# Performance work log

Measured on AMD Instinct MI355X. Metric: run time of the kernel, lower is better.

Reference implementation:

```python
import jax, jax.numpy as jnp
import numpy as np

B, C, H, W = 4, 256, 64, 64
CI = C // 2  # inter_channels = in_channels // 2
BN_EPS = 1e-5


def setup_inputs() -> dict:
    key = jax.random.key(0)
    ks = jax.random.split(key, 13)
    s = 0.02  # weight init scale for stability
    inp = {
        "x": jax.random.normal(ks[0], (B, C, H, W), dtype=jnp.float32),
        "w_theta": jax.random.normal(ks[1], (CI, C), dtype=jnp.float32) * s,
        "b_theta": jax.random.normal(ks[2], (CI,), dtype=jnp.float32) * s,
        "w_phi": jax.random.normal(ks[3], (CI, C), dtype=jnp.float32) * s,
        "b_phi": jax.random.normal(ks[4], (CI,), dtype=jnp.float32) * s,
        "w_g": jax.random.normal(ks[5], (CI, C), dtype=jnp.float32) * s,
        "b_g": jax.random.normal(ks[6], (CI,), dtype=jnp.float32) * s,
        "w_out": jax.random.normal(ks[7], (C, CI), dtype=jnp.float32) * s,
        "b_out": jax.random.normal(ks[8], (C,), dtype=jnp.float32) * s,
        "bn_gamma": jax.random.normal(ks[9], (C,), dtype=jnp.float32),
        "bn_beta": jax.random.normal(ks[10], (C,), dtype=jnp.float32) * s,
        "bn_mean": jax.random.normal(ks[11], (C,), dtype=jnp.float32) * s,
        "bn_var": jax.random.uniform(ks[12], (C,), dtype=jnp.float32, minval=0.5, maxval=1.5),
    }
    return inp


def _conv1x1(x, w, b):
    # 1x1 conv == channel contraction. x: [B,C,H,W], w: [O,C], b: [O]
    return jnp.einsum("bchw,oc->bohw", x, w) + b[None, :, None, None]


def reference(x, w_theta, b_theta, w_phi, b_phi, w_g, b_g,
              w_out, b_out, bn_gamma, bn_beta, bn_mean, bn_var):
    b, c, h, w = x.shape
    n = h * w
    # projections, flattened over spatial positions
    theta = _conv1x1(x, w_theta, b_theta).reshape(b, CI, n).transpose(0, 2, 1)  # [B,N,Ci]
    phi = _conv1x1(x, w_phi, b_phi).reshape(b, CI, n)                            # [B,Ci,N]
    g = _conv1x1(x, w_g, b_g).reshape(b, CI, n).transpose(0, 2, 1)               # [B,N,Ci]
    # unscaled dot-product attention over all spatial positions
    f = jnp.einsum("bnc,bcm->bnm", theta, phi)   # [B,N,N]
    attn = jax.nn.softmax(f, axis=-1)
    y = jnp.einsum("bnm,bmc->bnc", attn, g)      # [B,N,Ci]
    y = y.transpose(0, 2, 1).reshape(b, CI, h, w)
    # output 1x1 conv + BatchNorm (inference form) + residual
    wy = _conv1x1(y, w_out, b_out)
    inv = (bn_gamma / jnp.sqrt(bn_var + BN_EPS))[None, :, None, None]
    wy = (wy - bn_mean[None, :, None, None]) * inv + bn_beta[None, :, None, None]
    return wy + x
```

## Files before the change

kernel.cpp:

```cpp
#include <hip/hip_runtime.h>
#include <stdint.h>

#define NPOS 4096
#define NCH  256
#define NCI  128
#define NBATCH 4
#define NSPLIT 4
#define KRANGE (NPOS / NSPLIT)
#define LOG2E 1.44269504f

typedef float f32x16 __attribute__((ext_vector_type(16)));
typedef short short8 __attribute__((ext_vector_type(8)));

static __device__ __forceinline__ uint16_t f2bf(float f) {
  uint32_t u = __float_as_uint(f);
  u += 0x7fff + ((u >> 16) & 1);
  return (uint16_t)(u >> 16);
}
static __device__ __forceinline__ float bf2f(uint16_t h) {
  return __uint_as_float(((uint32_t)h) << 16);
}
static __device__ __forceinline__ uint32_t cvtpk(float a, float b) {
  uint32_t r;
  asm("v_cvt_pk_bf16_f32 %0, %1, %2" : "=v"(r) : "v"(a), "v"(b));
  return r;
}

__global__ void prep_kernel(const float* __restrict__ w_theta,
                            const float* __restrict__ w_phi,
                            const float* __restrict__ w_g,
                            const float* __restrict__ w_out,
                            const float* __restrict__ b_theta,
                            const float* __restrict__ b_phi,
                            const float* __restrict__ b_g,
                            const float* __restrict__ b_out,
                            const float* __restrict__ bn_gamma,
                            const float* __restrict__ bn_beta,
                            const float* __restrict__ bn_mean,
                            const float* __restrict__ bn_var,
                            uint16_t* __restrict__ w_all,
                            uint16_t* __restrict__ w_out_bf,
                            float* __restrict__ b_all,
                            float* __restrict__ bn_scale,
                            float* __restrict__ bn_shift) {
  int idx = blockIdx.x * 256 + threadIdx.x;
  if (idx < 98304) {
    int o = idx >> 8;
    float v;
    if (o < 128)      v = w_theta[idx] * LOG2E;
    else if (o < 256) v = w_phi[idx - 32768];
    else              v = w_g[idx - 65536];
    w_all[idx] = f2bf(v);
  } else if (idx < 131072) {
    w_out_bf[idx - 98304] = f2bf(w_out[idx - 98304]);
  } else if (idx < 131456) {
    int o = idx - 131072;
    float v = (o < 128) ? b_theta[o] * LOG2E
            : (o < 256) ? b_phi[o - 128] : b_g[o - 256];
    b_all[o] = v;
  } else if (idx < 131712) {
    int o = idx - 131456;
    float s = bn_gamma[o] * rsqrtf(bn_var[o] + 1e-5f);
    bn_scale[o] = s;
    bn_shift[o] = (b_out[o] - bn_mean[o]) * s + bn_beta[o];
  }
}

__global__ __launch_bounds__(512) void proj_kernel(
    const float* __restrict__ x, const uint16_t* __restrict__ w_all,
    const float* __restrict__ b_all,
    uint16_t* __restrict__ Q, uint16_t* __restrict__ K,
    uint16_t* __restrict__ Vt) {
  __shared__ __align__(16) uint16_t xs[64 * 256];
  int b = blockIdx.y;
  int n0 = blockIdx.x * 64;
  int tid = threadIdx.x;
  int lane = tid & 63;
  int wv = tid >> 6;
  const float* xb = x + ((size_t)b * NCH) * NPOS + n0;
  #pragma unroll
  for (int i = 0; i < 16; i++) {
    int c = wv * 32 + i * 2;
    float v0 = xb[(size_t)c * NPOS + lane];
    float v1 = xb[(size_t)(c + 1) * NPOS + lane];
    uint32_t u = cvtpk(v0, v1);
    *(uint32_t*)((char*)xs + lane * 512 + ((2 * c) ^ ((lane & 7) << 4))) = u;
  }
  __syncthreads();

  int l31 = lane & 31;
  int h2 = lane >> 5;
  int nt = wv & 1;
  int og = wv >> 1;
  int nl = nt * 32 + l31;
  int swz = (nl & 7) << 4;

  f32x16 accQ, accK, accV;
  #pragma unroll
  for (int i = 0; i < 16; i++) { accQ[i] = 0.f; accK[i] = 0.f; accV[i] = 0.f; }

  const uint16_t* wt = w_all + (size_t)(og * 32 + l31) * 256 + h2 * 8;
  const uint16_t* wp = wt + 128 * 256;
  const uint16_t* wg = wt + 256 * 256;

  #pragma unroll
  for (int kc = 0; kc < 16; kc++) {
    int c2 = kc * 32 + h2 * 16;
    short8 xf = *(const short8*)((const char*)xs + nl * 512 + (c2 ^ swz));
    short8 a = *(const short8*)(wt + kc * 16);
    short8 p = *(const short8*)(wp + kc * 16);
    short8 g = *(const short8*)(wg + kc * 16);
    accQ = __builtin_amdgcn_mfma_f32_32x32x16_bf16(xf, a, accQ, 0, 0, 0);
    accK = __builtin_amdgcn_mfma_f32_32x32x16_bf16(xf, p, accK, 0, 0, 0);
    accV = __builtin_amdgcn_mfma_f32_32x32x16_bf16(g, xf, accV, 0, 0, 0);
  }

  int ocol = og * 32 + l31;
  float bq = b_all[ocol];
  float bk = b_all[128 + ocol];
  #pragma unroll
  for (int r = 0; r < 16; r++) {
    int n = nt * 32 + (r & 3) + 8 * (r >> 2) + 4 * h2;
    size_t row = ((size_t)b * NPOS + n0 + n) * NCI + ocol;
    Q[row] = f2bf(accQ[r] + bq);
    K[row] = f2bf(accK[r] + bk);
  }
  #pragma unroll
  for (int r = 0; r < 16; r++) {
    int ci = og * 32 + (r & 3) + 8 * (r >> 2) + 4 * h2;
    Vt[((size_t)b * NCI + ci) * NPOS + n0 + nt * 32 + l31] =
        f2bf(accV[r] + b_all[256 + ci]);
  }
}

__global__ __launch_bounds__(256, 2) void attn_kernel(
    const uint16_t* __restrict__ Q, const uint16_t* __restrict__ K,
    const uint16_t* __restrict__ Vt, uint16_t* __restrict__ Ypart,
    float* __restrict__ Dpart) {
  __shared__ __align__(16) uint16_t kv[4 * 4096];
  uint16_t* Kb0 = kv;
  uint16_t* Vb0 = kv + 4096;
  uint16_t* Kb1 = kv + 8192;
  uint16_t* Vb1 = kv + 12288;

  int wg = blockIdx.x;
  int xcd = wg & 7;
  int slot = wg >> 3;
  int b = xcd >> 1;
  int split = (xcd & 1) * 2 + (slot & 1);
  int qblk = slot >> 1;
  int tid = threadIdx.x;
  int lane = tid & 63;
  int wv = tid >> 6;
  int q32 = lane & 31;
  int h2 = lane >> 5;
  int qb = qblk * 128 + wv * 32;

  const uint16_t* Qb = Q + ((size_t)b * NPOS + qb + q32) * NCI + h2 * 8;
  short8 qf[8];
  #pragma unroll
  for (int kc = 0; kc < 8; kc++)
    qf[kc] = *reinterpret_cast<const short8*>(Qb + kc * 16);

  const uint16_t* Kg = K + (size_t)b * NPOS * NCI;
  const uint16_t* Vg = Vt + (size_t)b * NCI * NPOS;

  int posA = wv * 2048 + lane * 16;
  int posB = posA + 1024;
  int rKA = posA >> 8, cKA = (posA >> 4) & 15;
  int rKB = posB >> 8, cKB = (posB >> 4) & 15;
  int wrKA = rKA * 128 + ((cKA ^ (rKA & 7)) << 3);
  int wrKB = rKB * 128 + ((cKB ^ (rKB & 7)) << 3);
  int gKA = rKA * NCI + cKA * 8;
  int gKB = rKB * NCI + cKB * 8;
  int ciA = posA >> 6, vsA = (posA >> 4) & 3;
  int ciB = posB >> 6, vsB = (posB >> 4) & 3;
  int wrVA = ciA * 32 + ((vsA ^ ((ciA >> 1) & 3)) << 3);
  int wrVB = ciB * 32 + ((vsB ^ ((ciB >> 1) & 3)) << 3);
  int gVA = ciA * NPOS + vsA * 8;
  int gVB = ciB * NPOS + vsB * 8;

  short8 stK0, stK1, stV0, stV1;

#define LOADR(MB)                                                             \
  {                                                                           \
    const uint16_t* kt = Kg + (size_t)(MB) * NCI;                             \
    const uint16_t* vt = Vg + (MB);                                           \
    stK0 = *(const short8*)(kt + gKA);                                        \
    stK1 = *(const short8*)(kt + gKB);                                        \
    stV0 = *(const short8*)(vt + gVA);                                        \
    stV1 = *(const short8*)(vt + gVB);                                        \
  }
#define WRITE(KB, VB)                                                         \
  {                                                                           \
    *(short8*)((KB) + wrKA) = stK0;                                           \
    *(short8*)((KB) + wrKB) = stK1;                                           \
    *(short8*)((VB) + wrVA) = stV0;                                           \
    *(short8*)((VB) + wrVB) = stV1;                                           \
  }

  f32x16 yacc[4];
  #pragma unroll
  for (int d = 0; d < 4; d++)
    #pragma unroll
    for (int i = 0; i < 16; i++) yacc[d][i] = 0.f;

  float den = 0.f;
  int m0 = split * KRANGE;

#define ATTN_BODY(KB, VB)                                                     \
  {                                                                           \
    short8 kf[8];                                                             \
    _Pragma("unroll")                                                         \
    for (int kc = 0; kc < 8; kc++) {                                          \
      int off = q32 * 128 + (((2 * kc + h2) ^ (q32 & 7)) << 3);               \
      kf[kc] = *(const short8*)((KB) + off);                                  \
    }                                                                         \
    short8 vf[2][4];                                                          \
    _Pragma("unroll")                                                         \
    for (int kc2 = 0; kc2 < 2; kc2++)                                         \
      _Pragma("unroll")                                                       \
      for (int dt = 0; dt < 4; dt++) {                                        \
        int ci = q32 + dt * 32;                                               \
        int off = ci * 32 + (((2 * kc2 + h2) ^ ((q32 >> 1) & 3)) << 3);       \
        vf[kc2][dt] = *(const short8*)((VB) + off);                           \
      }                                                                       \
    f32x16 s;                                                                 \
    _Pragma("unroll")                                                         \
    for (int i = 0; i < 16; i++) s[i] = 0.f;                                  \
    _Pragma("unroll")                                                         \
    for (int kc = 0; kc < 8; kc++)                                            \
      s = __builtin_amdgcn_mfma_f32_32x32x16_bf16(kf[kc], qf[kc], s, 0, 0, 0);\
    _Pragma("unroll")                                                         \
    for (int i = 0; i < 16; i++) s[i] = exp2f(s[i]);                          \
    float r0 = (s[0] + s[1]) + (s[2] + s[3]);                                 \
    float r1 = (s[4] + s[5]) + (s[6] + s[7]);                                 \
    float r2 = (s[8] + s[9]) + (s[10] + s[11]);                               \
    float r3 = (s[12] + s[13]) + (s[14] + s[15]);                             \
    den += (r0 + r1) + (r2 + r3);                                             \
    uint32_t pk[8];                                                           \
    _Pragma("unroll")                                                         \
    for (int a2 = 0; a2 < 4; a2++) {                                          \
      pk[a2 * 2]     = cvtpk(s[4 * a2],     s[4 * a2 + 1]);                   \
      pk[a2 * 2 + 1] = cvtpk(s[4 * a2 + 2], s[4 * a2 + 3]);                   \
    }                                                                         \
    _Pragma("unroll")                                                         \
    for (int kc2 = 0; kc2 < 2; kc2++) {                                       \
      uint32_t A0 = pk[4 * kc2],     B0 = pk[4 * kc2 + 2];                    \
      uint32_t A1 = pk[4 * kc2 + 1], B1 = pk[4 * kc2 + 3];                    \
      asm("v_permlane32_swap_b32 %0, %1" : "+v"(A0), "+v"(B0));               \
      asm("v_permlane32_swap_b32 %0, %1" : "+v"(A1), "+v"(B1));               \
      union { short8 v; uint32_t u[4]; } pb;                                  \
      pb.u[0] = A0;                                                           \
      pb.u[1] = A1;                                                           \
      pb.u[2] = B0;                                                           \
      pb.u[3] = B1;                                                           \
      _Pragma("unroll")                                                       \
      for (int dt = 0; dt < 4; dt++)                                          \
        yacc[dt] = __builtin_amdgcn_mfma_f32_32x32x16_bf16(vf[kc2][dt], pb.v, \
                                                           yacc[dt], 0, 0, 0);\
    }                                                                         \
  }

  LOADR(m0)
  WRITE(Kb0, Vb0)
  __syncthreads();

  for (int it = 0; it < 16; it++) {
    int ms = it * 64;
    LOADR(m0 + ms + 32)
    ATTN_BODY(Kb0, Vb0)
    WRITE(Kb1, Vb1)
    __syncthreads();
    int mn = m0 + ((ms + 64) & (KRANGE - 1));
    LOADR(mn)
    ATTN_BODY(Kb1, Vb1)
    WRITE(Kb0, Vb0)
    __syncthreads();
  }
#undef ATTN_BODY
#undef LOADR
#undef WRITE

  size_t pbase = ((size_t)(b * NSPLIT + split)) * NCI * NPOS;
  #pragma unroll
  for (int dt = 0; dt < 4; dt++)
    #pragma unroll
    for (int r = 0; r < 16; r++) {
      int drow = dt * 32 + (r & 3) + 8 * (r >> 2) + 4 * h2;
      Ypart[pbase + (size_t)drow * NPOS + qb + q32] = f2bf(yacc[dt][r]);
    }
  den += __shfl_xor(den, 32);
  if (h2 == 0) {
    size_t sbase = (size_t)(b * NSPLIT + split) * NPOS + qb + q32;
    Dpart[sbase] = den;
  }
}

__global__ __launch_bounds__(512) void out_kernel(
    const uint16_t* __restrict__ Yp, const float* __restrict__ Dp,
    const uint16_t* __restrict__ w_out_bf,
    const float* __restrict__ bn_scale, const float* __restrict__ bn_shift,
    const float* __restrict__ x, float* __restrict__ out) {
  __shared__ __align__(16) uint16_t ys[64 * 128];
  int b = blockIdx.y;
  int n0 = blockIdx.x * 64;
  int tid = threadIdx.x;
  int n = tid & 63;
  int wv = tid >> 6;

  float den = 0.f;
  #pragma unroll
  for (int s2 = 0; s2 < NSPLIT; s2++)
    den += Dp[(size_t)(b * NSPLIT + s2) * NPOS + n0 + n];
  float rden = 1.f / den;

  #pragma unroll
  for (int i = 0; i < 16; i += 2) {
    int ci0 = wv * 16 + i;
    float a0 = 0.f, a1 = 0.f;
    #pragma unroll
    for (int s2 = 0; s2 < NSPLIT; s2++) {
      size_t base = ((size_t)(b * NSPLIT + s2) * NCI) * NPOS + n0 + n;
      a0 += bf2f(Yp[base + (size_t)ci0 * NPOS]);
      a1 += bf2f(Yp[base + (size_t)(ci0 + 1) * NPOS]);
    }
    *(uint32_t*)((char*)ys + n * 256 + ((2 * ci0) ^ ((n & 7) << 4))) =
        cvtpk(a0 * rden, a1 * rden);
  }
  __syncthreads();

  int lane = tid & 63;
  int l31 = lane & 31;
  int h2 = lane >> 5;
  int og = wv;
  f32x16 acc0, acc1;
  #pragma unroll
  for (int i = 0; i < 16; i++) { acc0[i] = 0.f; acc1[i] = 0.f; }
  const uint16_t* wo_base = w_out_bf + (size_t)(og * 32 + l31) * NCI + h2 * 8;
  int swz = (l31 & 7) << 4;
  #pragma unroll
  for (int kc = 0; kc < 8; kc++) {
    int c2 = kc * 32 + h2 * 16;
    short8 wo = *(const short8*)(wo_base + kc * 16);
    short8 y0 = *(const short8*)((const char*)ys + l31 * 256 + (c2 ^ swz));
    short8 y1 = *(const short8*)((const char*)ys + (32 + l31) * 256 + (c2 ^ swz));
    acc0 = __builtin_amdgcn_mfma_f32_32x32x16_bf16(wo, y0, acc0, 0, 0, 0);
    acc1 = __builtin_amdgcn_mfma_f32_32x32x16_bf16(wo, y1, acc1, 0, 0, 0);
  }
  #pragma unroll
  for (int r = 0; r < 16; r++) {
    int o = og * 32 + (r & 3) + 8 * (r >> 2) + 4 * h2;
    float sc = bn_scale[o];
    float sh = bn_shift[o];
    size_t base = ((size_t)b * NCH + o) * NPOS + n0;
    out[base + l31]      = fmaf(acc0[r], sc, sh) + x[base + l31];
    out[base + 32 + l31] = fmaf(acc1[r], sc, sh) + x[base + 32 + l31];
  }
}

extern "C" void kernel_launch(void* const* d_in, const int* in_sizes, int n_in,
                              void* d_out, int out_size, void* d_ws, size_t ws_size,
                              hipStream_t stream) {
  const float* x        = (const float*)d_in[0];
  const float* w_theta  = (const float*)d_in[1];
  const float* b_theta  = (const float*)d_in[2];
  const float* w_phi    = (const float*)d_in[3];
  const float* b_phi    = (const float*)d_in[4];
  const float* w_g      = (const float*)d_in[5];
  const float* b_g      = (const float*)d_in[6];
  const float* w_out    = (const float*)d_in[7];
  const float* b_out    = (const float*)d_in[8];
  const float* bn_gamma = (const float*)d_in[9];
  const float* bn_beta  = (const float*)d_in[10];
  const float* bn_mean  = (const float*)d_in[11];
  const float* bn_var   = (const float*)d_in[12];

  char* ws = (char*)d_ws;
  uint16_t* w_all    = (uint16_t*)ws;  ws += (size_t)384 * 256 * 2;
  uint16_t* w_out_bf = (uint16_t*)ws;  ws += (size_t)256 * 128 * 2;
  float* b_all       = (float*)ws;     ws += 2048;
  float* bn_scale    = (float*)ws;     ws += 1024;
  float* bn_shift    = (float*)ws;     ws += 1024;
  uint16_t* Q   = (uint16_t*)ws;  ws += (size_t)NBATCH * NPOS * NCI * 2;
  uint16_t* Kb  = (uint16_t*)ws;  ws += (size_t)NBATCH * NPOS * NCI * 2;
  uint16_t* Vt  = (uint16_t*)ws;  ws += (size_t)NBATCH * NCI * NPOS * 2;
  uint16_t* Yp  = (uint16_t*)ws;  ws += (size_t)NBATCH * NSPLIT * NCI * NPOS * 2;
  float* Dp     = (float*)ws;     ws += (size_t)NBATCH * NSPLIT * NPOS * 4;

  hipLaunchKernelGGL(prep_kernel, dim3(515), dim3(256), 0, stream,
                     w_theta, w_phi, w_g, w_out, b_theta, b_phi, b_g, b_out,
                     bn_gamma, bn_beta, bn_mean, bn_var,
                     w_all, w_out_bf, b_all, bn_scale, bn_shift);
  hipLaunchKernelGGL(proj_kernel, dim3(64, NBATCH), dim3(512), 0, stream,
                     x, w_all, b_all, Q, Kb, Vt);
  hipLaunchKernelGGL(attn_kernel, dim3(512), dim3(256), 0, stream,
                     Q, Kb, Vt, Yp, Dp);
  hipLaunchKernelGGL(out_kernel, dim3(64, NBATCH), dim3(512), 0, stream,
                     Yp, Dp, w_out_bf, bn_scale, bn_shift, x, (float*)d_out);
}
```

Before: 156.9 us.

## Double key splits, raise attention occupancy, and vectorize partial reduction

Splits the key range of each batch's attention into 8 chunks instead of 4, doubling the attention grid and requesting 4 workgroups per CU via launch bounds. Wave priority is raised around the MFMA/softmax section to favor compute over loads. The output kernel now reduces the partial results with 16-byte vector loads, one channel row per thread group, and computes reciprocal denominators once into shared memory. This trades twice the partial-result memory traffic, and possible register spilling under the tighter register limit, for better latency hiding.

```diff
diff --git a/kernel.cpp b/kernel.cpp
--- a/kernel.cpp
+++ b/kernel.cpp
@@ -5,7 +5,7 @@
 #define NCH  256
 #define NCI  128
 #define NBATCH 4
-#define NSPLIT 4
+#define NSPLIT 8
 #define KRANGE (NPOS / NSPLIT)
 #define LOG2E 1.44269504f
 
@@ -133,7 +133,7 @@
   }
 }
 
-__global__ __launch_bounds__(256, 2) void attn_kernel(
+__global__ __launch_bounds__(256, 4) void attn_kernel(
     const uint16_t* __restrict__ Q, const uint16_t* __restrict__ K,
     const uint16_t* __restrict__ Vt, uint16_t* __restrict__ Ypart,
     float* __restrict__ Dpart) {
@@ -147,8 +147,8 @@
   int xcd = wg & 7;
   int slot = wg >> 3;
   int b = xcd >> 1;
-  int split = (xcd & 1) * 2 + (slot & 1);
-  int qblk = slot >> 1;
+  int split = (xcd & 1) * 4 + (slot & 3);
+  int qblk = slot >> 2;
   int tid = threadIdx.x;
   int lane = tid & 63;
   int wv = tid >> 6;
@@ -225,6 +225,7 @@
         int off = ci * 32 + (((2 * kc2 + h2) ^ ((q32 >> 1) & 3)) << 3);       \
         vf[kc2][dt] = *(const short8*)((VB) + off);                           \
       }                                                                       \
+    __builtin_amdgcn_s_setprio(1);                                            \
     f32x16 s;                                                                 \
     _Pragma("unroll")                                                         \
     for (int i = 0; i < 16; i++) s[i] = 0.f;                                  \
@@ -260,13 +261,14 @@
         yacc[dt] = __builtin_amdgcn_mfma_f32_32x32x16_bf16(vf[kc2][dt], pb.v, \
                                                            yacc[dt], 0, 0, 0);\
     }                                                                         \
+    __builtin_amdgcn_s_setprio(0);                                            \
   }
 
   LOADR(m0)
   WRITE(Kb0, Vb0)
   __syncthreads();
 
-  for (int it = 0; it < 16; it++) {
+  for (int it = 0; it < KRANGE / 64; it++) {
     int ms = it * 64;
     LOADR(m0 + ms + 32)
     ATTN_BODY(Kb0, Vb0)
@@ -303,34 +305,49 @@
     const float* __restrict__ bn_scale, const float* __restrict__ bn_shift,
     const float* __restrict__ x, float* __restrict__ out) {
   __shared__ __align__(16) uint16_t ys[64 * 128];
+  __shared__ float rden_s[64];
   int b = blockIdx.y;
   int n0 = blockIdx.x * 64;
   int tid = threadIdx.x;
-  int n = tid & 63;
+
+  if (tid < 64) {
+    float den = 0.f;
+    #pragma unroll
+    for (int s2 = 0; s2 < NSPLIT; s2++)
+      den += Dp[(size_t)(b * NSPLIT + s2) * NPOS + n0 + tid];
+    rden_s[tid] = 1.f / den;
+  }
+  __syncthreads();
+
+  {
+    int ci = tid >> 2;
+    int g = tid & 3;
+    float sum[16];
+    #pragma unroll
+    for (int j = 0; j < 16; j++) sum[j] = 0.f;
+    #pragma unroll
+    for (int s2 = 0; s2 < NSPLIT; s2++) {
+      const uint16_t* p =
+          Yp + ((size_t)(b * NSPLIT + s2) * NCI + ci) * NPOS + n0 + g * 16;
+      short8 v0 = *(const short8*)(p);
+      short8 v1 = *(const short8*)(p + 8);
+      #pragma unroll
+      for (int j = 0; j < 8; j++) {
+        sum[j]     += bf2f((uint16_t)v0[j]);
+        sum[8 + j] += bf2f((uint16_t)v1[j]);
+      }
+    }
+    #pragma unroll
+    for (int j = 0; j < 16; j++) {
+      int n = g * 16 + j;
+      float v = sum[j] * rden_s[n];
+      *(uint16_t*)((char*)ys + n * 256 + ((2 * ci) ^ ((n & 7) << 4))) = f2bf(v);
+    }
+  }
+  __syncthreads();
+
+  int lane = tid & 63;
   int wv = tid >> 6;
-
-  float den = 0.f;
-  #pragma unroll
-  for (int s2 = 0; s2 < NSPLIT; s2++)
-    den += Dp[(size_t)(b * NSPLIT + s2) * NPOS + n0 + n];
-  float rden = 1.f / den;
-
-  #pragma unroll
-  for (int i = 0; i < 16; i += 2) {
-    int ci0 = wv * 16 + i;
-    float a0 = 0.f, a1 = 0.f;
-    #pragma unroll
-    for (int s2 = 0; s2 < NSPLIT; s2++) {
-      size_t base = ((size_t)(b * NSPLIT + s2) * NCI) * NPOS + n0 + n;
-      a0 += bf2f(Yp[base + (size_t)ci0 * NPOS]);
-      a1 += bf2f(Yp[base + (size_t)(ci0 + 1) * NPOS]);
-    }
-    *(uint32_t*)((char*)ys + n * 256 + ((2 * ci0) ^ ((n & 7) << 4))) =
-        cvtpk(a0 * rden, a1 * rden);
-  }
-  __syncthreads();
-
-  int lane = tid & 63;
   int l31 = lane & 31;
   int h2 = lane >> 5;
   int og = wv;
@@ -394,7 +411,7 @@
                      w_all, w_out_bf, b_all, bn_scale, bn_shift);
   hipLaunchKernelGGL(proj_kernel, dim3(64, NBATCH), dim3(512), 0, stream,
                      x, w_all, b_all, Q, Kb, Vt);
-  hipLaunchKernelGGL(attn_kernel, dim3(512), dim3(256), 0, stream,
+  hipLaunchKernelGGL(attn_kernel, dim3(1024), dim3(256), 0, stream,
                      Q, Kb, Vt, Yp, Dp);
   hipLaunchKernelGGL(out_kernel, dim3(64, NBATCH), dim3(512), 0, stream,
                      Yp, Dp, w_out_bf, bn_scale, bn_shift, x, (float*)d_out);
```

After: 528.4 us. 237% more time.
